# Kernel tuning notes

Measured on AMD Instinct MI355X. Metric: run time of the kernel, lower is better.

Reference implementation:

```python
import jax, jax.numpy as jnp
import numpy as np

SIZE = 1024
INPUT_SIZE = 1024
CONTEXT_SIZE = 512
CMS = 6            # context_map_size -> 2**6 = 64 weight slots per neuron
BATCH = 128
LR = 0.01
OUT_CLIP = 0.01
W_CLIP = 5.0


def setup_inputs() -> dict:
    key = jax.random.key(0)
    k1, k2, k3, k4, k5, k6 = jax.random.split(key, 6)
    logits = jax.random.normal(k1, (INPUT_SIZE, BATCH), dtype=jnp.float32)
    context_inputs = jax.random.normal(k2, (CONTEXT_SIZE, BATCH), dtype=jnp.float32)
    targets = jax.random.uniform(k3, (BATCH,), dtype=jnp.float32)
    # learned/fixed parameters (GLN params are non-trainable buffers in torch)
    projection = 0.1 * jax.random.normal(k4, (SIZE, CMS, CONTEXT_SIZE), dtype=jnp.float32)
    projection = projection / jnp.linalg.norm(projection, axis=2, keepdims=True)
    projection_bias = 0.1 * jax.random.normal(k5, (SIZE, CMS, 1), dtype=jnp.float32)
    weights = jnp.full((SIZE, 2 ** CMS, INPUT_SIZE), 1.0 / INPUT_SIZE, dtype=jnp.float32)
    bias = jax.random.uniform(k6, (), dtype=jnp.float32, minval=OUT_CLIP, maxval=1.0 - OUT_CLIP)
    return {"logits": logits, "context_inputs": context_inputs, "targets": targets,
            "projection": projection, "projection_bias": projection_bias,
            "weights": weights, "bias": bias}


def reference(logits, context_inputs, targets, projection, projection_bias, weights, bias):
    # context hashing: (size,cms,ctx) @ (ctx,batch) -> (size,cms,batch)
    projected = jnp.einsum('smc,cb->smb', projection, context_inputs)
    bits = (projected > projection_bias).astype(jnp.int32)
    bool_conv = (2 ** jnp.arange(CMS, dtype=jnp.int32))[None, :, None]  # (1,cms,1)
    ctx_idx = jnp.sum(bits * bool_conv, axis=1)  # (size, batch) in [0, 2**cms)
    # gather per-(neuron, sample) weight rows: (size, batch, input_size)
    sel_w = jnp.take_along_axis(weights, ctx_idx[:, :, None], axis=1)
    # batched dot (torch does full matmul + diagonal; same math, done directly)
    out = jnp.einsum('sbi,ib->sb', sel_w, logits)  # (size, batch)
    out = out.at[0].set(bias)  # bias neuron overwrites row 0
    # online weight update + scatter back
    sigmoids = jnp.clip(jax.nn.sigmoid(out), OUT_CLIP, 1.0 - OUT_CLIP)
    upd = LR * (sigmoids - targets[None, :])[:, :, None] * logits.T[None, :, :]  # (size,batch,input)
    new_sel = jnp.clip(sel_w - upd, -W_CLIP, W_CLIP)
    rows = jnp.arange(SIZE)[:, None]
    new_weights = weights.at[rows, ctx_idx].set(new_sel)
    return jnp.squeeze(out), new_weights
```

## Files before the change

kernel.cpp:

```cpp
#include <hip/hip_runtime.h>

#define GLN_SIZE 1024
#define GLN_INPUT 1024
#define GLN_CTX 512
#define GLN_CMS 6
#define GLN_NCTX 64
#define GLN_BATCH 128
#define GLN_LR 0.01f
#define GLN_OUT_CLIP 0.01f
#define GLN_W_CLIP 5.0f

typedef float f32x4 __attribute__((ext_vector_type(4)));

__global__ __launch_bounds__(256) void transpose_kernel(
    const float* __restrict__ in, float* __restrict__ out, int R, int C)
{
    __shared__ float tile[32][33];
    const int bx = blockIdx.x * 32;
    const int by = blockIdx.y * 32;
    const int tx = threadIdx.x;
    const int ty = threadIdx.y;
#pragma unroll
    for (int j = 0; j < 32; j += 8)
        tile[ty + j][tx] = in[(by + ty + j) * C + (bx + tx)];
    __syncthreads();
#pragma unroll
    for (int j = 0; j < 32; j += 8)
        out[(bx + ty + j) * R + (by + tx)] = tile[tx][ty + j];
}

__global__ __launch_bounds__(128) void hash_kernel(
    const float* __restrict__ ctxT,
    const float* __restrict__ proj,
    const float* __restrict__ pbias,
    int* __restrict__ idx)
{
    const int s = blockIdx.x;
    const int b = threadIdx.x;

    const f32x4* ct = (const f32x4*)(ctxT + (size_t)b * GLN_CTX);
    const f32x4* pr = (const f32x4*)(proj + (size_t)s * GLN_CMS * GLN_CTX);

    float acc[GLN_CMS] = {0.f, 0.f, 0.f, 0.f, 0.f, 0.f};
    for (int c4 = 0; c4 < GLN_CTX / 4; ++c4) {
        f32x4 v = ct[c4];
#pragma unroll
        for (int m = 0; m < GLN_CMS; ++m) {
            f32x4 p = pr[m * (GLN_CTX / 4) + c4];
            acc[m] += p[0] * v[0];
            acc[m] += p[1] * v[1];
            acc[m] += p[2] * v[2];
            acc[m] += p[3] * v[3];
        }
    }
    int v = 0;
#pragma unroll
    for (int m = 0; m < GLN_CMS; ++m)
        v |= (acc[m] > pbias[s * GLN_CMS + m]) ? (1 << m) : 0;
    idx[s * GLN_BATCH + b] = v;
}

__device__ __forceinline__ float dot_row(const f32x4* __restrict__ lg,
                                         const f32x4 w4[4], int lane)
{
    float p = 0.f;
#pragma unroll
    for (int k = 0; k < 4; ++k) {
        f32x4 g = lg[lane + k * 64];
        p += w4[k][0] * g[0] + w4[k][1] * g[1] +
             w4[k][2] * g[2] + w4[k][3] * g[3];
    }
#pragma unroll
    for (int off = 1; off < 64; off <<= 1)
        p += __shfl_xor(p, off, 64);
    return p;
}

__device__ __forceinline__ void dot_row2(const f32x4* __restrict__ la,
                                         const f32x4* __restrict__ lb,
                                         const f32x4 w4[4], int lane,
                                         float& pa, float& pb)
{
    float a = 0.f, b = 0.f;
#pragma unroll
    for (int k = 0; k < 4; ++k) {
        f32x4 ga = la[lane + k * 64];
        f32x4 gb = lb[lane + k * 64];
        a += w4[k][0] * ga[0] + w4[k][1] * ga[1] +
             w4[k][2] * ga[2] + w4[k][3] * ga[3];
        b += w4[k][0] * gb[0] + w4[k][1] * gb[1] +
             w4[k][2] * gb[2] + w4[k][3] * gb[3];
    }
#pragma unroll
    for (int off = 1; off < 64; off <<= 1) {
        a += __shfl_xor(a, off, 64);
        b += __shfl_xor(b, off, 64);
    }
    pa = a; pb = b;
}

__device__ __forceinline__ float delta_of(float outval, float tgt)
{
    float sg = 1.0f / (1.0f + expf(-outval));
    sg = fminf(fmaxf(sg, GLN_OUT_CLIP), 1.0f - GLN_OUT_CLIP);
    return GLN_LR * (sg - tgt);
}

__global__ __launch_bounds__(256) void gln_kernel(
    const float* __restrict__ weights,
    const float* __restrict__ logitsT,
    const float* __restrict__ targets,
    const float* __restrict__ biasPtr,
    const int* __restrict__ idx,
    float* __restrict__ outv,
    float* __restrict__ outw)
{
    const int s    = blockIdx.x >> 1;
    const int half = blockIdx.x & 1;
    const int tid  = threadIdx.x;
    const int lane = tid & 63;
    const int wv   = tid >> 6;

    __shared__ int cnt[GLN_NCTX];
    __shared__ int winner[GLN_NCTX];
    __shared__ unsigned char lists[GLN_NCTX][GLN_BATCH];

    if (tid < GLN_NCTX) { cnt[tid] = 0; winner[tid] = -1; }
    __syncthreads();
    if (tid < GLN_BATCH) {
        int c = idx[s * GLN_BATCH + tid];
        int slot = atomicAdd(&cnt[c], 1);
        lists[c][slot] = (unsigned char)tid;
        atomicMax(&winner[c], tid);
    }
    __syncthreads();

    const float bias = biasPtr[0];
    const float* wrow_base = weights + (size_t)s * GLN_NCTX * GLN_INPUT;
    float*       orow_base = outw    + (size_t)s * GLN_NCTX * GLN_INPUT;
    const int rowbase = half * 32 + wv * 8;

    f32x4 w4[4], w4n[4];
    {
        const f32x4* wr = (const f32x4*)(wrow_base + rowbase * GLN_INPUT);
#pragma unroll
        for (int k = 0; k < 4; ++k) w4[k] = wr[lane + k * 64];
    }

#pragma unroll
    for (int ci = 0; ci < 8; ++ci) {
        const int c = rowbase + ci;

        if (ci < 7) {
            const f32x4* wrn = (const f32x4*)(wrow_base + (c + 1) * GLN_INPUT);
#pragma unroll
            for (int k = 0; k < 4; ++k) w4n[k] = wrn[lane + k * 64];
        }

        const int n    = cnt[c];
        const int bwin = winner[c];
        float dwin = 0.0f;

        int u = 0;
        for (; u + 1 < n; u += 2) {
            const int ba = lists[c][u];
            const int bb = lists[c][u + 1];
            float oa, ob;
            if (s != 0) {
                dot_row2((const f32x4*)(logitsT + ba * GLN_INPUT),
                         (const f32x4*)(logitsT + bb * GLN_INPUT),
                         w4, lane, oa, ob);
            } else {
                oa = bias; ob = bias;
            }
            float da = delta_of(oa, targets[ba]);
            float db = delta_of(ob, targets[bb]);
            if (lane == 0) {
                outv[s * GLN_BATCH + ba] = oa;
                outv[s * GLN_BATCH + bb] = ob;
            }
            if (ba == bwin) dwin = da;
            if (bb == bwin) dwin = db;
        }
        if (u < n) {
            const int b = lists[c][u];
            float outval;
            if (s != 0)
                outval = dot_row((const f32x4*)(logitsT + b * GLN_INPUT), w4, lane);
            else
                outval = bias;
            float d = delta_of(outval, targets[b]);
            if (lane == 0) outv[s * GLN_BATCH + b] = outval;
            if (b == bwin) dwin = d;
        }

        f32x4* orow = (f32x4*)(orow_base + c * GLN_INPUT);
        if (bwin >= 0) {
            const f32x4* lg = (const f32x4*)(logitsT + bwin * GLN_INPUT);
#pragma unroll
            for (int k = 0; k < 4; ++k) {
                f32x4 g = lg[lane + k * 64];
                f32x4 r;
                r[0] = fminf(fmaxf(w4[k][0] - dwin * g[0], -GLN_W_CLIP), GLN_W_CLIP);
                r[1] = fminf(fmaxf(w4[k][1] - dwin * g[1], -GLN_W_CLIP), GLN_W_CLIP);
                r[2] = fminf(fmaxf(w4[k][2] - dwin * g[2], -GLN_W_CLIP), GLN_W_CLIP);
                r[3] = fminf(fmaxf(w4[k][3] - dwin * g[3], -GLN_W_CLIP), GLN_W_CLIP);
                __builtin_nontemporal_store(r, orow + lane + k * 64);
            }
        } else {
#pragma unroll
            for (int k = 0; k < 4; ++k)
                __builtin_nontemporal_store(w4[k], orow + lane + k * 64);
        }

#pragma unroll
        for (int k = 0; k < 4; ++k) w4[k] = w4n[k];
    }
}

extern "C" void kernel_launch(void* const* d_in, const int* in_sizes, int n_in,
                              void* d_out, int out_size, void* d_ws, size_t ws_size,
                              hipStream_t stream) {
    const float* logits  = (const float*)d_in[0];
    const float* ctx     = (const float*)d_in[1];
    const float* targets = (const float*)d_in[2];
    const float* proj    = (const float*)d_in[3];
    const float* pbias   = (const float*)d_in[4];
    const float* weights = (const float*)d_in[5];
    const float* bias    = (const float*)d_in[6];

    float* outv = (float*)d_out;
    float* outw = outv + GLN_SIZE * GLN_BATCH;

    float* logitsT = (float*)d_ws;
    float* ctxT    = logitsT + GLN_BATCH * GLN_INPUT;
    int*   idx     = (int*)(ctxT + GLN_BATCH * GLN_CTX);

    transpose_kernel<<<dim3(GLN_BATCH / 32, GLN_INPUT / 32), dim3(32, 8), 0, stream>>>(
        logits, logitsT, GLN_INPUT, GLN_BATCH);
    transpose_kernel<<<dim3(GLN_BATCH / 32, GLN_CTX / 32), dim3(32, 8), 0, stream>>>(
        ctx, ctxT, GLN_CTX, GLN_BATCH);
    hash_kernel<<<GLN_SIZE, 128, 0, stream>>>(ctxT, proj, pbias, idx);
    gln_kernel<<<GLN_SIZE * 2, 256, 0, stream>>>(weights, logitsT, targets, bias,
                                                 idx, outv, outw);
}
```

Measured before the change: 531.7 us.

## Replace shared-memory context bucketing with per-wave ballot masks and finer work split

Each wave now handles two context rows of one neuron instead of eight. It finds the matching samples with wave-wide ballots over the context indices rather than building shared-memory lists with atomics and block barriers. The grid grows fourfold so more waves are in flight to hide the latency of the 256 MB weight stream. The cost is that every wave reloads the neuron's 128 indices and does ballot and bit-scan work, and there is less prefetch pipelining across rows within a wave.

```diff
diff --git a/kernel.cpp b/kernel.cpp
--- a/kernel.cpp
+++ b/kernel.cpp
@@ -115,56 +115,52 @@
     float* __restrict__ outv,
     float* __restrict__ outw)
 {
-    const int s    = blockIdx.x >> 1;
-    const int half = blockIdx.x & 1;
     const int tid  = threadIdx.x;
     const int lane = tid & 63;
     const int wv   = tid >> 6;
-
-    __shared__ int cnt[GLN_NCTX];
-    __shared__ int winner[GLN_NCTX];
-    __shared__ unsigned char lists[GLN_NCTX][GLN_BATCH];
-
-    if (tid < GLN_NCTX) { cnt[tid] = 0; winner[tid] = -1; }
-    __syncthreads();
-    if (tid < GLN_BATCH) {
-        int c = idx[s * GLN_BATCH + tid];
-        int slot = atomicAdd(&cnt[c], 1);
-        lists[c][slot] = (unsigned char)tid;
-        atomicMax(&winner[c], tid);
-    }
-    __syncthreads();
+    const int unit = blockIdx.x * 4 + wv;
+    const int s    = unit >> 5;
+    const int c0   = (unit & 31) * 2;
+
+    const int i0 = idx[s * GLN_BATCH + lane];
+    const int i1 = idx[s * GLN_BATCH + 64 + lane];
 
     const float bias = biasPtr[0];
     const float* wrow_base = weights + (size_t)s * GLN_NCTX * GLN_INPUT;
     float*       orow_base = outw    + (size_t)s * GLN_NCTX * GLN_INPUT;
-    const int rowbase = half * 32 + wv * 8;
 
     f32x4 w4[4], w4n[4];
     {
-        const f32x4* wr = (const f32x4*)(wrow_base + rowbase * GLN_INPUT);
+        const f32x4* wr = (const f32x4*)(wrow_base + c0 * GLN_INPUT);
 #pragma unroll
         for (int k = 0; k < 4; ++k) w4[k] = wr[lane + k * 64];
     }
 
 #pragma unroll
-    for (int ci = 0; ci < 8; ++ci) {
-        const int c = rowbase + ci;
-
-        if (ci < 7) {
+    for (int ci = 0; ci < 2; ++ci) {
+        const int c = c0 + ci;
+
+        if (ci == 0) {
             const f32x4* wrn = (const f32x4*)(wrow_base + (c + 1) * GLN_INPUT);
 #pragma unroll
             for (int k = 0; k < 4; ++k) w4n[k] = wrn[lane + k * 64];
         }
 
-        const int n    = cnt[c];
-        const int bwin = winner[c];
+        unsigned long long m0 = __ballot(i0 == c);
+        unsigned long long m1 = __ballot(i1 == c);
+        int bwin = -1;
+        if (m1)      bwin = 64 + 63 - __builtin_clzll(m1);
+        else if (m0) bwin = 63 - __builtin_clzll(m0);
         float dwin = 0.0f;
 
-        int u = 0;
-        for (; u + 1 < n; u += 2) {
-            const int ba = lists[c][u];
-            const int bb = lists[c][u + 1];
+        int n = __popcll(m0) + __popcll(m1);
+        while (n >= 2) {
+            int ba, bb;
+            if (m0) { ba = __builtin_ctzll(m0); m0 &= m0 - 1; }
+            else    { ba = 64 + __builtin_ctzll(m1); m1 &= m1 - 1; }
+            if (m0) { bb = __builtin_ctzll(m0); m0 &= m0 - 1; }
+            else    { bb = 64 + __builtin_ctzll(m1); m1 &= m1 - 1; }
+            n -= 2;
             float oa, ob;
             if (s != 0) {
                 dot_row2((const f32x4*)(logitsT + ba * GLN_INPUT),
@@ -182,8 +178,10 @@
             if (ba == bwin) dwin = da;
             if (bb == bwin) dwin = db;
         }
-        if (u < n) {
-            const int b = lists[c][u];
+        if (n == 1) {
+            int b;
+            if (m0) b = __builtin_ctzll(m0);
+            else    b = 64 + __builtin_ctzll(m1);
             float outval;
             if (s != 0)
                 outval = dot_row((const f32x4*)(logitsT + b * GLN_INPUT), w4, lane);
@@ -241,6 +239,6 @@
     transpose_kernel<<<dim3(GLN_BATCH / 32, GLN_CTX / 32), dim3(32, 8), 0, stream>>>(
         ctx, ctxT, GLN_CTX, GLN_BATCH);
     hash_kernel<<<GLN_SIZE, 128, 0, stream>>>(ctxT, proj, pbias, idx);
-    gln_kernel<<<GLN_SIZE * 2, 256, 0, stream>>>(weights, logitsT, targets, bias,
+    gln_kernel<<<GLN_SIZE * 8, 256, 0, stream>>>(weights, logitsT, targets, bias,
                                                  idx, outv, outw);
 }
```

Measured after the change: 513.7 us. 1.04x faster.
